# Performance work log

Hardware: AMD Instinct MI355X
Metric: run time of the kernel (lower is better)

## Reference

```python
import jax, jax.numpy as jnp
import numpy as np

N_NODES = 50000
N_EDGES = 800000
D_IN = 128
D_OUT = 128


def setup_inputs() -> dict:
    key = jax.random.key(0)
    k = jax.random.split(key, 6)
    x = jax.random.normal(k[0], (N_NODES, D_IN), dtype=jnp.float32)
    weight = jax.random.normal(k[1], (D_IN, D_OUT), dtype=jnp.float32) * (1.0 / np.sqrt(D_IN))
    bias = jax.random.normal(k[2], (D_OUT,), dtype=jnp.float32)
    src = jax.random.randint(k[3], (N_EDGES,), 0, N_NODES, dtype=jnp.int32)
    dst = jax.random.randint(k[4], (N_EDGES,), 0, N_NODES, dtype=jnp.int32)
    edge_vals = jax.random.uniform(k[5], (N_EDGES,), dtype=jnp.float32)
    return {"x": x, "weight": weight, "bias": bias, "src": src, "dst": dst, "edge_vals": edge_vals}


def reference(x, weight, bias, src, dst, edge_vals):
    # support = x @ W  (dense projection), [N, D_OUT]
    support = jnp.matmul(x, weight)
    # spmm: out[d] = sum_{e: dst[e]==d} edge_vals[e] * support[src[e]]
    msgs = support[src] * edge_vals[:, None]  # [E, D_OUT]
    out = jax.ops.segment_sum(msgs, dst, num_segments=x.shape[0])
    return out + bias
```

## Files before the change

kernel.cpp:

```cpp
#include <hip/hip_runtime.h>
#include <hip/hip_bf16.h>

#define D 128
#define BKT 64
#define CAP 1536
#define SC_EPB 8192
#define NBMAX 800

typedef __attribute__((ext_vector_type(8))) short bf16x8;
typedef __attribute__((ext_vector_type(4))) float f32x4;

__device__ __forceinline__ unsigned short f2bf(float f) {
  union { float f; unsigned u; } c; c.f = f;
  unsigned u = c.u + 0x7FFFu + ((c.u >> 16) & 1u);
  return (unsigned short)(u >> 16);
}
__device__ __forceinline__ float bf_lo(unsigned u) {
  union { unsigned u; float f; } c; c.u = u << 16; return c.f;
}
__device__ __forceinline__ float bf_hi(unsigned u) {
  union { unsigned u; float f; } c; c.u = u & 0xFFFF0000u; return c.f;
}

__global__ __launch_bounds__(256) void conv_wT(
    const float* __restrict__ w, unsigned short* __restrict__ wT) {
  const int idx = blockIdx.x * 256 + threadIdx.x;
  const int k = idx >> 7, n = idx & 127;
  wT[n * D + k] = f2bf(w[idx]);
}

__global__ __launch_bounds__(256) void gemm_xw_mfma(
    const float* __restrict__ x, const unsigned short* __restrict__ wT,
    unsigned short* __restrict__ supb, int n_nodes) {
  __shared__ unsigned short xs[64 * 136];

  const int tid = threadIdx.x;
  const int row0 = blockIdx.x * 64;

  for (int f = tid; f < 64 * 32; f += 256) {
    const int r = f >> 5, c4 = f & 31;
    const int gr = row0 + r;
    float4 v = make_float4(0.f, 0.f, 0.f, 0.f);
    if (gr < n_nodes) v = ((const float4*)(x + (size_t)gr * D))[c4];
    ushort4 b;
    b.x = f2bf(v.x); b.y = f2bf(v.y); b.z = f2bf(v.z); b.w = f2bf(v.w);
    *(ushort4*)(&xs[r * 136 + c4 * 4]) = b;
  }
  __syncthreads();

  const int wv = tid >> 6;
  const int lane = tid & 63;
  const int l15 = lane & 15;
  const int quad = lane >> 4;

  f32x4 acc[8];
#pragma unroll
  for (int t = 0; t < 8; t++) acc[t] = (f32x4){0.f, 0.f, 0.f, 0.f};

#pragma unroll
  for (int k0 = 0; k0 < D; k0 += 32) {
    const bf16x8 a = *(const bf16x8*)(&xs[(wv * 16 + l15) * 136 + k0 + quad * 8]);
    const unsigned short* wp = wT + (size_t)l15 * D + k0 + quad * 8;
#pragma unroll
    for (int t = 0; t < 8; t++) {
      const bf16x8 b = *(const bf16x8*)(wp + (size_t)t * 16 * D);
      acc[t] = __builtin_amdgcn_mfma_f32_16x16x32_bf16(a, b, acc[t], 0, 0, 0);
    }
  }

#pragma unroll
  for (int t = 0; t < 8; t++) {
    const int col = t * 16 + l15;
#pragma unroll
    for (int r = 0; r < 4; r++) {
      const int row = row0 + wv * 16 + quad * 4 + r;
      if (row < n_nodes) supb[(size_t)row * D + col] = f2bf(acc[t][r]);
    }
  }
}

__global__ __launch_bounds__(512) void bucket_scatter(
    const int* __restrict__ src, const int* __restrict__ dst,
    const float* __restrict__ ev, int* __restrict__ bcur,
    uint2* __restrict__ staged, int n_edges, int nb) {
  __shared__ int hist[NBMAX];
  __shared__ int cur[NBMAX];
  const int t = threadIdx.x;
  const int base = blockIdx.x * SC_EPB;
  const int cnt = min(SC_EPB, n_edges - base);

  for (int i = t; i < nb; i += 512) hist[i] = 0;
  __syncthreads();
  for (int j = t; j < cnt; j += 512) atomicAdd(&hist[dst[base + j] >> 6], 1);
  __syncthreads();
  for (int i = t; i < nb; i += 512) {
    const int h = hist[i];
    cur[i] = h ? atomicAdd(&bcur[i], h) : 0;
  }
  __syncthreads();
  for (int j = t; j < cnt; j += 512) {
    const int e = base + j;
    const int d = dst[e];
    const int b = d >> 6;
    const int p = atomicAdd(&cur[b], 1);
    if (p < CAP) {
      staged[(size_t)b * CAP + p] =
          make_uint2((unsigned)src[e] | ((unsigned)(d & 63) << 16),
                     (unsigned)__float_as_int(ev[e]));
    }
  }
}

__global__ __launch_bounds__(512) void bucket_reduce(
    const unsigned short* __restrict__ supb, const uint2* __restrict__ staged,
    const int* __restrict__ bcnt, const float* __restrict__ bias,
    float* __restrict__ out, int n_nodes) {
  __shared__ uint2 rec[CAP];
  __shared__ uint2 ordered[CAP];
  __shared__ int hist[BKT];
  __shared__ int segbase[BKT];
  __shared__ int cur[BKT];

  const int t = threadIdx.x;
  const int b = blockIdx.x;
  const int lo = b << 6;
  const int cnt = min(bcnt[b], CAP);
  const uint2* st = staged + (size_t)b * CAP;

  if (t < BKT) hist[t] = 0;
  __syncthreads();
  for (int j = t; j < cnt; j += 512) {
    const uint2 p = st[j];
    rec[j] = p;
    atomicAdd(&hist[p.x >> 16], 1);
  }
  __syncthreads();
  if (t == 0) {
    int run = 0;
    for (int i = 0; i < BKT; i++) {
      segbase[i] = run;
      cur[i] = run;
      run += hist[i];
    }
  }
  __syncthreads();
  for (int j = t; j < cnt; j += 512) {
    const uint2 p = rec[j];
    const int pos = atomicAdd(&cur[p.x >> 16], 1);
    ordered[pos] = p;
  }
  __syncthreads();

  const int n = t >> 3;
  const int p = t & 7;
  const int beg = segbase[n];
  const int end = beg + hist[n];

  float a[16];
#pragma unroll
  for (int k = 0; k < 16; k++) a[k] = 0.f;

  for (int j = beg; j < end; j++) {
    const uint2 pr = ordered[j];
    const int s = pr.x & 0xFFFF;
    const float v = __int_as_float((int)pr.y);
    const uint4* row = (const uint4*)(supb + (size_t)s * D) + p * 2;
    const uint4 r0 = row[0];
    const uint4 r1 = row[1];
    a[0]  += v * bf_lo(r0.x);  a[1]  += v * bf_hi(r0.x);
    a[2]  += v * bf_lo(r0.y);  a[3]  += v * bf_hi(r0.y);
    a[4]  += v * bf_lo(r0.z);  a[5]  += v * bf_hi(r0.z);
    a[6]  += v * bf_lo(r0.w);  a[7]  += v * bf_hi(r0.w);
    a[8]  += v * bf_lo(r1.x);  a[9]  += v * bf_hi(r1.x);
    a[10] += v * bf_lo(r1.y);  a[11] += v * bf_hi(r1.y);
    a[12] += v * bf_lo(r1.z);  a[13] += v * bf_hi(r1.z);
    a[14] += v * bf_lo(r1.w);  a[15] += v * bf_hi(r1.w);
  }

  const int node = lo + n;
  if (node < n_nodes) {
    const float4* bp = (const float4*)bias + p * 4;
    float4* op = (float4*)out + (size_t)node * 32 + p * 4;
#pragma unroll
    for (int q = 0; q < 4; q++) {
      const float4 bv = bp[q];
      op[q] = make_float4(a[q * 4 + 0] + bv.x, a[q * 4 + 1] + bv.y,
                          a[q * 4 + 2] + bv.z, a[q * 4 + 3] + bv.w);
    }
  }
}

extern "C" void kernel_launch(void* const* d_in, const int* in_sizes, int n_in,
                              void* d_out, int out_size, void* d_ws, size_t ws_size,
                              hipStream_t stream) {
  const float* x    = (const float*)d_in[0];
  const float* w    = (const float*)d_in[1];
  const float* bias = (const float*)d_in[2];
  const int*   src  = (const int*)d_in[3];
  const int*   dst  = (const int*)d_in[4];
  const float* ev   = (const float*)d_in[5];
  float* out = (float*)d_out;

  const int n_nodes = in_sizes[0] / D;
  const int n_edges = in_sizes[3];
  const int nb = (n_nodes + BKT - 1) / BKT;

  unsigned short* supb = (unsigned short*)d_ws;
  unsigned short* wT = supb + (size_t)n_nodes * D;
  int* bcur = (int*)(wT + D * D);
  uint2* staged = (uint2*)(bcur + NBMAX);

  hipMemsetAsync(bcur, 0, nb * sizeof(int), stream);

  bucket_scatter<<<(n_edges + SC_EPB - 1) / SC_EPB, 512, 0, stream>>>(
      src, dst, ev, bcur, staged, n_edges, nb);

  conv_wT<<<(D * D + 255) / 256, 256, 0, stream>>>(w, wT);
  gemm_xw_mfma<<<(n_nodes + 63) / 64, 256, 0, stream>>>(x, wT, supb, n_nodes);

  bucket_reduce<<<nb, 512, 0, stream>>>(supb, staged, bcur, bias, out, n_nodes);
}
```

Measured before the change: 169.6 us.

## Fuse weight conversion with counter reset and widen reduce to 1024 threads

Merges the weight transpose/convert kernel and the bucket counter memset into one setup launch, removing a separate memset and kernel. The scatter kernel processes fewer edges per block, which gives more blocks and more parallelism. The reduce kernel now runs 1024 threads with 16 lanes per node, each handling 8 features, and unrolls the edge loop by two so two row gathers are in flight at once. It also replaces the serial single-thread prefix sum with a wavefront shuffle scan. The larger block may lower occupancy, and more scatter blocks means more global atomics on the bucket counters.

```diff
diff --git a/kernel.cpp b/kernel.cpp
--- a/kernel.cpp
+++ b/kernel.cpp
@@ -4,7 +4,7 @@
 #define D 128
 #define BKT 64
 #define CAP 1536
-#define SC_EPB 8192
+#define SC_EPB 4096
 #define NBMAX 800
 
 typedef __attribute__((ext_vector_type(8))) short bf16x8;
@@ -22,11 +22,15 @@
   union { unsigned u; float f; } c; c.u = u & 0xFFFF0000u; return c.f;
 }
 
-__global__ __launch_bounds__(256) void conv_wT(
-    const float* __restrict__ w, unsigned short* __restrict__ wT) {
+__global__ __launch_bounds__(256) void setup(
+    const float* __restrict__ w, unsigned short* __restrict__ wT,
+    int* __restrict__ bcur, int nb) {
   const int idx = blockIdx.x * 256 + threadIdx.x;
-  const int k = idx >> 7, n = idx & 127;
-  wT[n * D + k] = f2bf(w[idx]);
+  if (idx < D * D) {
+    const int k = idx >> 7, n = idx & 127;
+    wT[n * D + k] = f2bf(w[idx]);
+  }
+  if (idx < nb) bcur[idx] = 0;
 }
 
 __global__ __launch_bounds__(256) void gemm_xw_mfma(
@@ -111,7 +115,7 @@
   }
 }
 
-__global__ __launch_bounds__(512) void bucket_reduce(
+__global__ __launch_bounds__(1024) void bucket_reduce(
     const unsigned short* __restrict__ supb, const uint2* __restrict__ staged,
     const int* __restrict__ bcnt, const float* __restrict__ bias,
     float* __restrict__ out, int n_nodes) {
@@ -129,64 +133,78 @@
 
   if (t < BKT) hist[t] = 0;
   __syncthreads();
-  for (int j = t; j < cnt; j += 512) {
+  for (int j = t; j < cnt; j += 1024) {
     const uint2 p = st[j];
     rec[j] = p;
     atomicAdd(&hist[p.x >> 16], 1);
   }
   __syncthreads();
-  if (t == 0) {
-    int run = 0;
-    for (int i = 0; i < BKT; i++) {
-      segbase[i] = run;
-      cur[i] = run;
-      run += hist[i];
-    }
-  }
-  __syncthreads();
-  for (int j = t; j < cnt; j += 512) {
+  if (t < BKT) {
+    const int h = hist[t];
+    int incl = h;
+#pragma unroll
+    for (int ofs = 1; ofs < 64; ofs <<= 1) {
+      const int v = __shfl_up(incl, ofs, 64);
+      if (t >= ofs) incl += v;
+    }
+    segbase[t] = incl - h;
+    cur[t] = incl - h;
+  }
+  __syncthreads();
+  for (int j = t; j < cnt; j += 1024) {
     const uint2 p = rec[j];
     const int pos = atomicAdd(&cur[p.x >> 16], 1);
     ordered[pos] = p;
   }
   __syncthreads();
 
-  const int n = t >> 3;
-  const int p = t & 7;
+  const int n = t >> 4;
+  const int p = t & 15;
   const int beg = segbase[n];
   const int end = beg + hist[n];
 
-  float a[16];
-#pragma unroll
-  for (int k = 0; k < 16; k++) a[k] = 0.f;
-
-  for (int j = beg; j < end; j++) {
-    const uint2 pr = ordered[j];
-    const int s = pr.x & 0xFFFF;
-    const float v = __int_as_float((int)pr.y);
-    const uint4* row = (const uint4*)(supb + (size_t)s * D) + p * 2;
-    const uint4 r0 = row[0];
-    const uint4 r1 = row[1];
-    a[0]  += v * bf_lo(r0.x);  a[1]  += v * bf_hi(r0.x);
-    a[2]  += v * bf_lo(r0.y);  a[3]  += v * bf_hi(r0.y);
-    a[4]  += v * bf_lo(r0.z);  a[5]  += v * bf_hi(r0.z);
-    a[6]  += v * bf_lo(r0.w);  a[7]  += v * bf_hi(r0.w);
-    a[8]  += v * bf_lo(r1.x);  a[9]  += v * bf_hi(r1.x);
-    a[10] += v * bf_lo(r1.y);  a[11] += v * bf_hi(r1.y);
-    a[12] += v * bf_lo(r1.z);  a[13] += v * bf_hi(r1.z);
-    a[14] += v * bf_lo(r1.w);  a[15] += v * bf_hi(r1.w);
+  float a[8];
+#pragma unroll
+  for (int k = 0; k < 8; k++) a[k] = 0.f;
+
+  int j = beg;
+  for (; j + 2 <= end; j += 2) {
+    const uint2 pr0 = ordered[j];
+    const uint2 pr1 = ordered[j + 1];
+    const uint4 r0 = ((const uint4*)(supb + (size_t)(pr0.x & 0xFFFF) * D))[p];
+    const uint4 r1 = ((const uint4*)(supb + (size_t)(pr1.x & 0xFFFF) * D))[p];
+    const float v0 = __int_as_float((int)pr0.y);
+    const float v1 = __int_as_float((int)pr1.y);
+    a[0] += v0 * bf_lo(r0.x) + v1 * bf_lo(r1.x);
+    a[1] += v0 * bf_hi(r0.x) + v1 * bf_hi(r1.x);
+    a[2] += v0 * bf_lo(r0.y) + v1 * bf_lo(r1.y);
+    a[3] += v0 * bf_hi(r0.y) + v1 * bf_hi(r1.y);
+    a[4] += v0 * bf_lo(r0.z) + v1 * bf_lo(r1.z);
+    a[5] += v0 * bf_hi(r0.z) + v1 * bf_hi(r1.z);
+    a[6] += v0 * bf_lo(r0.w) + v1 * bf_lo(r1.w);
+    a[7] += v0 * bf_hi(r0.w) + v1 * bf_hi(r1.w);
+  }
+  if (j < end) {
+    const uint2 pr0 = ordered[j];
+    const uint4 r0 = ((const uint4*)(supb + (size_t)(pr0.x & 0xFFFF) * D))[p];
+    const float v0 = __int_as_float((int)pr0.y);
+    a[0] += v0 * bf_lo(r0.x);
+    a[1] += v0 * bf_hi(r0.x);
+    a[2] += v0 * bf_lo(r0.y);
+    a[3] += v0 * bf_hi(r0.y);
+    a[4] += v0 * bf_lo(r0.z);
+    a[5] += v0 * bf_hi(r0.z);
+    a[6] += v0 * bf_lo(r0.w);
+    a[7] += v0 * bf_hi(r0.w);
   }
 
   const int node = lo + n;
   if (node < n_nodes) {
-    const float4* bp = (const float4*)bias + p * 4;
-    float4* op = (float4*)out + (size_t)node * 32 + p * 4;
-#pragma unroll
-    for (int q = 0; q < 4; q++) {
-      const float4 bv = bp[q];
-      op[q] = make_float4(a[q * 4 + 0] + bv.x, a[q * 4 + 1] + bv.y,
-                          a[q * 4 + 2] + bv.z, a[q * 4 + 3] + bv.w);
-    }
+    const float4 bv0 = ((const float4*)bias)[p * 2];
+    const float4 bv1 = ((const float4*)bias)[p * 2 + 1];
+    float4* op = (float4*)out + (size_t)node * 32 + p * 2;
+    op[0] = make_float4(a[0] + bv0.x, a[1] + bv0.y, a[2] + bv0.z, a[3] + bv0.w);
+    op[1] = make_float4(a[4] + bv1.x, a[5] + bv1.y, a[6] + bv1.z, a[7] + bv1.w);
   }
 }
 
@@ -210,13 +228,12 @@
   int* bcur = (int*)(wT + D * D);
   uint2* staged = (uint2*)(bcur + NBMAX);
 
-  hipMemsetAsync(bcur, 0, nb * sizeof(int), stream);
+  setup<<<64, 256, 0, stream>>>(w, wT, bcur, nb);
 
   bucket_scatter<<<(n_edges + SC_EPB - 1) / SC_EPB, 512, 0, stream>>>(
       src, dst, ev, bcur, staged, n_edges, nb);
 
-  conv_wT<<<(D * D + 255) / 256, 256, 0, stream>>>(w, wT);
   gemm_xw_mfma<<<(n_nodes + 63) / 64, 256, 0, stream>>>(x, wT, supb, n_nodes);
 
-  bucket_reduce<<<nb, 512, 0, stream>>>(supb, staged, bcur, bias, out, n_nodes);
-}
+  bucket_reduce<<<nb, 1024, 0, stream>>>(supb, staged, bcur, bias, out, n_nodes);
+}
```

Result: faster. 153.0 us (-9.8%).
